# Kernel tuning notes

Measured on AMD Instinct MI355X. Metric: run time of the kernel, lower is better.

The kernel has to match this reference:

```python
import jax, jax.numpy as jnp
import numpy as np

B = 4096      # batch
IN = 512      # input_size
HS = [256, 128, 64]  # hidden_sizes (num liquid neurons per layer)
S = 64        # liquid_state_size
OUT = 12      # output_size


def setup_inputs() -> dict:
    key = jax.random.key(0)
    keys = iter(jax.random.split(key, 40))

    def rn(shape, scale=0.05):
        return jax.random.normal(next(keys), shape, dtype=jnp.float32) * scale

    inp = {"x": jax.random.normal(next(keys), (B, IN), dtype=jnp.float32)}
    sizes = [IN] + HS
    for l, (din, n) in enumerate(zip(sizes[:-1], sizes[1:])):
        inp[f"Wi{l}"] = rn((n, din, S))   # stacked input_projection weights
        inp[f"bi{l}"] = rn((n, S))        # input_projection biases
        inp[f"bl{l}"] = rn((n, S))        # liquid_state biases (hidden starts at 0)
        inp[f"Wo{l}"] = rn((n, S))        # output_projection weights (out dim 1)
        inp[f"bo{l}"] = rn((n,))          # output_projection biases
        inp[f"L{l}"]  = rn((n, n), 0.1)   # lateral_weights
        inp[f"a{l}"]  = jnp.ones((n,), jnp.float32)  # adaptation_state
    inp["Wout"] = rn((HS[-1], OUT))
    inp["bout"] = rn((OUT,))
    return inp


def _liquid_layer(x, Wi, bi, bl, Wo, bo, L, a):
    # Stacked over neurons n: liquid_input[b,n,s] = x @ Wi_n + bi_n + bl_n
    li = jnp.einsum('bi,nis->bns', x, Wi) + bi[None] + bl[None]
    act = jnp.tanh(li) + 0.1 * jnp.sin(0.5 * li) * jnp.cos(0.3 * li)
    # per-neuron scalar output projection -> [B, N]
    out = jnp.einsum('bns,ns->bn', act, Wo) + bo
    # lateral mixing + adaptation scaling
    out = out + 0.1 * (out @ L)
    return out * a


def reference(x, Wi0, bi0, bl0, Wo0, bo0, L0, a0,
              Wi1, bi1, bl1, Wo1, bo1, L1, a1,
              Wi2, bi2, bl2, Wo2, bo2, L2, a2,
              Wout, bout):
    h = _liquid_layer(x, Wi0, bi0, bl0, Wo0, bo0, L0, a0)
    h = _liquid_layer(h, Wi1, bi1, bl1, Wo1, bo1, L1, a1)
    h = _liquid_layer(h, Wi2, bi2, bl2, Wo2, bo2, L2, a2)
    return h @ Wout + bout
```

## Files before the change

### kernel.cpp

```cpp
#include <hip/hip_runtime.h>
#include <hip/hip_bf16.h>
#include <math.h>


#define BATCH 4096

typedef __bf16 bf16x8 __attribute__((ext_vector_type(8)));
typedef float floatx4 __attribute__((ext_vector_type(4)));

__device__ __forceinline__ void gl_lds16(const void* g, void* l) {
    __builtin_amdgcn_global_load_lds(
        (const __attribute__((address_space(1))) void*)g,
        (__attribute__((address_space(3))) void*)l, 16, 0, 0);
}

__device__ __forceinline__ float act_exact(float v) {
    return tanhf(v) + 0.1f * sinf(0.5f * v) * cosf(0.3f * v);
}


__device__ __forceinline__ void wconv_tile(const float* __restrict__ Wi,
                                           __hip_bfloat16* __restrict__ Wt,
                                           int K, int n, int k0, int t)
{
    __shared__ float lds[64][65];
    const float* src = Wi + ((size_t)n * K + k0) * 64;
#pragma unroll
    for (int i = 0; i < 4; ++i) {
        int idx = t + i * 256;
        int r = idx >> 4;
        int s4 = (idx & 15) * 4;
        float4 v = *(const float4*)(src + (size_t)r * 64 + s4);
        lds[s4 + 0][r] = v.x;
        lds[s4 + 1][r] = v.y;
        lds[s4 + 2][r] = v.z;
        lds[s4 + 3][r] = v.w;
    }
    __syncthreads();
    __hip_bfloat16* dst = Wt + (size_t)n * 64 * K + k0;
#pragma unroll
    for (int i = 0; i < 4; ++i) {
        int idx = t + i * 256;
        int s = idx >> 4;
        int k4 = (idx & 15) * 4;
        union { ushort4 u4; __hip_bfloat16 b[4]; } o;
        o.b[0] = __float2bfloat16(lds[s][k4 + 0]);
        o.b[1] = __float2bfloat16(lds[s][k4 + 1]);
        o.b[2] = __float2bfloat16(lds[s][k4 + 2]);
        o.b[3] = __float2bfloat16(lds[s][k4 + 3]);
        *(ushort4*)(dst + (size_t)s * K + k4) = o.u4;
    }
}

__global__ __launch_bounds__(256) void conv_all(
    const float* __restrict__ x, __hip_bfloat16* __restrict__ xb,
    const float* __restrict__ Wi0, const float* __restrict__ Wi1,
    const float* __restrict__ Wi2,
    __hip_bfloat16* __restrict__ Wt0, __hip_bfloat16* __restrict__ Wt1,
    __hip_bfloat16* __restrict__ Wt2, float* __restrict__ Tg)
{
    int bid = blockIdx.x;
    int t = threadIdx.x;
    if (bid < 2048) {
        int g = bid * 256 + t;
        float4 v = ((const float4*)x)[g];
        union { ushort4 u4; __hip_bfloat16 b[4]; } o;
        o.b[0] = __float2bfloat16(v.x);
        o.b[1] = __float2bfloat16(v.y);
        o.b[2] = __float2bfloat16(v.z);
        o.b[3] = __float2bfloat16(v.w);
        ((ushort4*)xb)[g] = o.u4;
    } else if (bid < 4096) {
        int r = bid - 2048;
        wconv_tile(Wi0, Wt0, 512, r >> 3, (r & 7) * 64, t);
    } else if (bid < 4608) {
        int r = bid - 4096;
        wconv_tile(Wi1, Wt1, 256, r >> 2, (r & 3) * 64, t);
    } else if (bid < 4736) {
        int r = bid - 4608;
        wconv_tile(Wi2, Wt2, 128, r >> 1, (r & 1) * 64, t);
    } else {
#pragma unroll
        for (int i = 0; i < 2; ++i) {
            int e = t + 256 * i;
            float v0 = (float)(e - 256) * 0.03125f;
            Tg[2 * e] = act_exact(v0);
            Tg[2 * e + 1] = act_exact(v0 + 0.03125f);
        }
    }
}


__global__ __launch_bounds__(512, 4) void liquid_proj_mfma(
    const __hip_bfloat16* __restrict__ X,
    const __hip_bfloat16* __restrict__ Wt,
    const float* __restrict__ bi, const float* __restrict__ bl,
    const float* __restrict__ Wo, const float* __restrict__ bo,
    const float* __restrict__ Tg,
    __hip_bfloat16* __restrict__ t, int K, int Nn)
{
    __shared__ __align__(16) __hip_bfloat16 As[128 * 64];
    __shared__ __align__(16) __hip_bfloat16 Bs[256 * 64];
    __shared__ __align__(16) float Tt[1024];

    const int tid = threadIdx.x;
    const int wid = tid >> 6;
    const int wb = wid & 1;
    const int wn = wid >> 1;
    const int lane = tid & 63;
    const int m = lane & 15;
    const int qd = lane >> 4;

    const int bid = blockIdx.x;
    const int xcd = bid & 7;
    const int sw = bid >> 3;
    const int n_grp = sw >> 2;
    const int row_grp = ((sw & 3) << 3) | xcd;
    const int row0 = row_grp * 128;
    const int n0 = n_grp * 4;
    const int n = n0 + wn;

    if (tid < 256)
        gl_lds16(Tg + tid * 4, (void*)(Tt + tid * 4));

    floatx4 acc[4][4];
#pragma unroll
    for (int rt = 0; rt < 4; ++rt) {
        int sb = n * 64 + rt * 16 + qd * 4;
        float4 b4i = *(const float4*)(bi + sb);
        float4 b4l = *(const float4*)(bl + sb);
        floatx4 b4 = {b4i.x + b4l.x, b4i.y + b4l.y, b4i.z + b4l.z, b4i.w + b4l.w};
#pragma unroll
        for (int ct = 0; ct < 4; ++ct)
            acc[rt][ct] = b4;
    }

    const int ar0 = tid >> 3;
    const int aq0 = (tid & 7) ^ (ar0 & 7);
    const int ar1 = (tid + 512) >> 3;
    const int aq1 = ((tid + 512) & 7) ^ (ar1 & 7);
    const __hip_bfloat16* Xr0 = X + (size_t)(row0 + ar0) * K + aq0 * 8;
    const __hip_bfloat16* Xr1 = X + (size_t)(row0 + ar1) * K + aq1 * 8;

    const __hip_bfloat16* bsrc[4];
#pragma unroll
    for (int i = 0; i < 4; ++i) {
        int Li = i * 512 + tid;
        int c = Li >> 3;
        int q = (Li & 7) ^ (c & 7);
        bsrc[i] = Wt + ((size_t)(n0 + (c >> 6)) * 64 + (c & 63)) * K + q * 8;
    }

    for (int k0 = 0; k0 < K; k0 += 64) {
        gl_lds16(Xr0 + k0, (void*)(As + tid * 8));
        gl_lds16(Xr1 + k0, (void*)(As + ((size_t)tid + 512) * 8));
#pragma unroll
        for (int i = 0; i < 4; ++i)
            gl_lds16(bsrc[i] + k0, (void*)(Bs + ((size_t)i * 512 + tid) * 8));
        __syncthreads();
#pragma unroll
        for (int kk = 0; kk < 2; ++kk) {
            bf16x8 af[4], bfr[4];
#pragma unroll
            for (int rt = 0; rt < 4; ++rt) {
                int sr = wn * 64 + rt * 16 + m;
                int slot = sr * 8 + ((kk * 4 + qd) ^ (sr & 7));
                af[rt] = *(const bf16x8*)(Bs + slot * 8);
            }
#pragma unroll
            for (int ct = 0; ct < 4; ++ct) {
                int br = wb * 64 + ct * 16 + m;
                int slot = br * 8 + ((kk * 4 + qd) ^ (br & 7));
                bfr[ct] = *(const bf16x8*)(As + slot * 8);
            }
#pragma unroll
            for (int rt = 0; rt < 4; ++rt)
#pragma unroll
                for (int ct = 0; ct < 4; ++ct)
                    acc[rt][ct] = __builtin_amdgcn_mfma_f32_16x16x32_bf16(
                        af[rt], bfr[ct], acc[rt][ct], 0, 0, 0);
        }
        __syncthreads();
    }

    float wo[4][4];
#pragma unroll
    for (int rt = 0; rt < 4; ++rt) {
        float4 w4 = *(const float4*)(Wo + n * 64 + rt * 16 + qd * 4);
        wo[rt][0] = w4.x; wo[rt][1] = w4.y; wo[rt][2] = w4.z; wo[rt][3] = w4.w;
    }
    float bov = bo[n];
    float p[4] = {0.f, 0.f, 0.f, 0.f};
    const float2* Tt2 = (const float2*)Tt;
#pragma unroll
    for (int ct = 0; ct < 4; ++ct)
#pragma unroll
        for (int rt = 0; rt < 4; ++rt)
#pragma unroll
            for (int reg = 0; reg < 4; ++reg) {
                float v = acc[rt][ct][reg];
                float u = fmaf(v, 32.f, 256.f);
                u = fminf(fmaxf(u, 0.f), 510.99f);
                float fi = floorf(u);
                int ii = (int)fi;
                float fr = u - fi;
                float2 pr = Tt2[ii];
                p[ct] = fmaf(fmaf(fr, pr.y - pr.x, pr.x), wo[rt][reg], p[ct]);
            }
#pragma unroll
    for (int ct = 0; ct < 4; ++ct) {
        p[ct] += __shfl_xor(p[ct], 16, 64);
        p[ct] += __shfl_xor(p[ct], 32, 64);
    }
    if (qd == 0) {
#pragma unroll
        for (int ct = 0; ct < 4; ++ct)
            t[(size_t)(row0 + wb * 64 + ct * 16 + m) * Nn + n] =
                __float2bfloat16(p[ct] + bov);
    }
}


template <int NN, int NNSH, bool FINAL>
__global__ __launch_bounds__(256) void lateral_fused(
    const __hip_bfloat16* __restrict__ t,
    const float* __restrict__ Lm,
    const float* __restrict__ a,
    __hip_bfloat16* __restrict__ h,
    const float* __restrict__ Wout,
    const float* __restrict__ bout,
    float* __restrict__ y)
{
    constexpr int RPT = NN / 16;
    __shared__ float tbT[NN][20];
    __shared__ float hb[16][65];

    const int tid = threadIdx.x;
    const int row0 = blockIdx.x * 16;

#pragma unroll
    for (int i = 0; i < NN / 16; ++i) {
        int idx = tid + i * 256;
        int r = idx >> NNSH;
        int c = idx & (NN - 1);
        tbT[c][r] = __bfloat162float(t[(size_t)(row0 + r) * NN + c]);
    }
    __syncthreads();

    const int c = tid & (NN - 1);
    const int rb = (tid >> NNSH) * RPT;
    float acc[RPT];
#pragma unroll
    for (int r = 0; r < RPT; ++r) acc[r] = 0.f;

    for (int mm = 0; mm < NN; ++mm) {
        float lv = Lm[mm * NN + c];
#pragma unroll
        for (int rr = 0; rr < RPT / 4; ++rr) {
            float4 tv = *(const float4*)&tbT[mm][rb + 4 * rr];
            acc[4 * rr + 0] += tv.x * lv;
            acc[4 * rr + 1] += tv.y * lv;
            acc[4 * rr + 2] += tv.z * lv;
            acc[4 * rr + 3] += tv.w * lv;
        }
    }
    float av = a[c];
#pragma unroll
    for (int r = 0; r < RPT; ++r) {
        float hv = (tbT[c][rb + r] + 0.1f * acc[r]) * av;
        if constexpr (FINAL) {
            hb[rb + r][c] = hv;
        } else {
            h[(size_t)(row0 + rb + r) * NN + c] = __float2bfloat16(hv);
        }
    }
    if constexpr (FINAL) {
        __syncthreads();
        if (tid < 192) {
            int r = tid / 12, o = tid - 12 * r;
            float accy = bout[o];
#pragma unroll
            for (int k = 0; k < 64; ++k)
                accy += hb[r][k] * Wout[k * 12 + o];
            y[(size_t)(row0 + r) * 12 + o] = accy;
        }
    }
}


__global__ __launch_bounds__(256) void liquid_proj_f32(
    const float* __restrict__ x, const float* __restrict__ Wi,
    const float* __restrict__ bi, const float* __restrict__ bl,
    const float* __restrict__ Wo, const float* __restrict__ bo,
    float* __restrict__ t, int K, int Nn)
{
    __shared__ float xs[16][65];
    __shared__ float ws[16][65];
    const int tid = threadIdx.x;
    const int tx = tid & 15, ty = tid >> 4;
    const int row0 = blockIdx.x * 64;
    const int n = blockIdx.y;
    const float* Wn = Wi + (size_t)n * K * 64;
    float acc[4][4] = {};
    for (int k0 = 0; k0 < K; k0 += 16) {
#pragma unroll
        for (int i = 0; i < 4; ++i) {
            int li = tid + 256 * i;
            xs[li & 15][li >> 4] = x[(size_t)(row0 + (li >> 4)) * K + k0 + (li & 15)];
        }
#pragma unroll
        for (int i = 0; i < 4; ++i) {
            int li = tid + 256 * i;
            ws[li >> 6][li & 63] = Wn[(size_t)(k0 + (li >> 6)) * 64 + (li & 63)];
        }
        __syncthreads();
#pragma unroll
        for (int kk = 0; kk < 16; ++kk) {
            float xa[4], wb[4];
#pragma unroll
            for (int i = 0; i < 4; ++i) xa[i] = xs[kk][4 * ty + i];
#pragma unroll
            for (int j = 0; j < 4; ++j) wb[j] = ws[kk][4 * tx + j];
#pragma unroll
            for (int i = 0; i < 4; ++i)
#pragma unroll
                for (int j = 0; j < 4; ++j) acc[i][j] += xa[i] * wb[j];
        }
        __syncthreads();
    }
    float part[4] = {0.f, 0.f, 0.f, 0.f};
#pragma unroll
    for (int j = 0; j < 4; ++j) {
        int cc = 4 * tx + j;
        float bias = bi[n * 64 + cc] + bl[n * 64 + cc];
        float wov = Wo[n * 64 + cc];
#pragma unroll
        for (int i = 0; i < 4; ++i) {
            float v = acc[i][j] + bias;
            part[i] += (tanhf(v) + 0.1f * sinf(0.5f * v) * cosf(0.3f * v)) * wov;
        }
    }
#pragma unroll
    for (int mk = 1; mk < 16; mk <<= 1)
#pragma unroll
        for (int i = 0; i < 4; ++i) part[i] += __shfl_xor(part[i], mk, 64);
    if (tx == 0) {
        float b = bo[n];
#pragma unroll
        for (int i = 0; i < 4; ++i)
            t[(size_t)(row0 + 4 * ty + i) * Nn + n] = part[i] + b;
    }
}

__global__ void lateral_f32_kernel(const float* __restrict__ t,
                                   const float* __restrict__ L,
                                   const float* __restrict__ a,
                                   float* __restrict__ h, int Nn)
{
    extern __shared__ float tb[];
    const int b = blockIdx.x;
    const int n = threadIdx.x;
    tb[n] = t[(size_t)b * Nn + n];
    __syncthreads();
    float acc = 0.f;
    for (int mm = 0; mm < Nn; ++mm)
        acc += tb[mm] * L[(size_t)mm * Nn + n];
    h[(size_t)b * Nn + n] = (tb[n] + 0.1f * acc) * a[n];
}

__global__ void out_f32_kernel(const float* __restrict__ h,
                               const float* __restrict__ Wout,
                               const float* __restrict__ bout,
                               float* __restrict__ y)
{
    int g = blockIdx.x * blockDim.x + threadIdx.x;
    if (g >= BATCH * 12) return;
    int b = g / 12, o = g - 12 * b;
    float acc = bout[o];
    const float* hb = h + (size_t)b * 64;
#pragma unroll
    for (int k = 0; k < 64; ++k) acc += hb[k] * Wout[k * 12 + o];
    y[g] = acc;
}

extern "C" void kernel_launch(void* const* d_in, const int* in_sizes, int n_in,
                              void* d_out, int out_size, void* d_ws, size_t ws_size,
                              hipStream_t stream)
{
    (void)in_sizes; (void)n_in; (void)out_size;
    const float* x = (const float*)d_in[0];
    const float* Wout = (const float*)d_in[22];
    const float* bout = (const float*)d_in[23];
    const int dims[4] = {512, 256, 128, 64};
    char* ws = (char*)d_ws;
    const size_t MB = 1024u * 1024u;

    if (ws_size >= 28 * MB) {
        __hip_bfloat16* Wt0 = (__hip_bfloat16*)ws;
        __hip_bfloat16* Wt1 = (__hip_bfloat16*)(ws + 16 * MB);
        __hip_bfloat16* Wt2 = (__hip_bfloat16*)(ws + 20 * MB);
        __hip_bfloat16* Wts[3] = {Wt0, Wt1, Wt2};
        __hip_bfloat16* xb = (__hip_bfloat16*)(ws + 21 * MB);
        __hip_bfloat16* h0 = xb;
        __hip_bfloat16* h1 = (__hip_bfloat16*)(ws + 23 * MB);
        __hip_bfloat16* tbuf = (__hip_bfloat16*)(ws + 25 * MB);
        float* Tg = (float*)(ws + 27 * MB);

        conv_all<<<4737, 256, 0, stream>>>(
            x, xb, (const float*)d_in[1], (const float*)d_in[8],
            (const float*)d_in[15], Wt0, Wt1, Wt2, Tg);

        const __hip_bfloat16* prev = xb;
        const __hip_bfloat16* hbuf[3] = {h0, h1, nullptr};
        for (int l = 0; l < 3; ++l) {
            const float* bi = (const float*)d_in[1 + 7 * l + 1];
            const float* bl = (const float*)d_in[1 + 7 * l + 2];
            const float* Wo = (const float*)d_in[1 + 7 * l + 3];
            const float* bo = (const float*)d_in[1 + 7 * l + 4];
            const float* L  = (const float*)d_in[1 + 7 * l + 5];
            const float* a  = (const float*)d_in[1 + 7 * l + 6];
            const int K = dims[l], Nn = dims[l + 1];

            liquid_proj_mfma<<<32 * (Nn / 4), 512, 0, stream>>>(
                prev, Wts[l], bi, bl, Wo, bo, Tg, tbuf, K, Nn);
            if (l == 0)
                lateral_fused<256, 8, false><<<BATCH / 16, 256, 0, stream>>>(
                    tbuf, L, a, h0, nullptr, nullptr, nullptr);
            else if (l == 1)
                lateral_fused<128, 7, false><<<BATCH / 16, 256, 0, stream>>>(
                    tbuf, L, a, h1, nullptr, nullptr, nullptr);
            else
                lateral_fused<64, 6, true><<<BATCH / 16, 256, 0, stream>>>(
                    tbuf, L, a, nullptr, Wout, bout, (float*)d_out);
            prev = hbuf[l];
        }
    } else {
        float* tbufs[3] = {(float*)ws, (float*)ws, (float*)(ws + 4 * MB)};
        float* hs[3] = {(float*)(ws + 4 * MB), (float*)(ws + 2 * MB),
                        (float*)(ws + 5 * MB)};
        const float* prev = x;
        for (int l = 0; l < 3; ++l) {
            const float* Wi = (const float*)d_in[1 + 7 * l + 0];
            const float* bi = (const float*)d_in[1 + 7 * l + 1];
            const float* bl = (const float*)d_in[1 + 7 * l + 2];
            const float* Wo = (const float*)d_in[1 + 7 * l + 3];
            const float* bo = (const float*)d_in[1 + 7 * l + 4];
            const float* L  = (const float*)d_in[1 + 7 * l + 5];
            const float* a  = (const float*)d_in[1 + 7 * l + 6];
            const int K = dims[l], Nn = dims[l + 1];
            liquid_proj_f32<<<dim3(BATCH / 64, Nn), 256, 0, stream>>>(
                prev, Wi, bi, bl, Wo, bo, tbufs[l], K, Nn);
            lateral_f32_kernel<<<BATCH, Nn, Nn * sizeof(float), stream>>>(
                tbufs[l], L, a, hs[l], Nn);
            prev = hs[l];
        }
        out_f32_kernel<<<(BATCH * 12 + 255) / 256, 256, 0, stream>>>(
            hs[2], Wout, bout, (float*)d_out);
    }
}
```

Baseline: 268.5 us.

## Double-buffer projection GEMM with 256-row tiles and phased async LDS loads

Replaces the projection MFMA kernel with a templated version that works on 256 batch rows per block instead of 128, doubling per-warp accumulators to 4x8. Each block keeps two LDS stages and issues the global-to-LDS loads for the next K tile in quarters, interleaved with MFMA phases. It uses explicit vmcnt waits, barriers and setprio, so memory latency overlaps compute and the number of X reloads across neuron groups drops. In exchange, LDS and register use per block rises (occupancy bound lowered to 2), the grid gets smaller, and the hand-tuned barrier and waitcnt choreography is fragile.

```diff
diff --git a/kernel.cpp b/kernel.cpp
--- a/kernel.cpp
+++ b/kernel.cpp
@@ -91,16 +91,18 @@
 }
 
 
-__global__ __launch_bounds__(512, 4) void liquid_proj_mfma(
+template <int KT>
+__global__ __launch_bounds__(512, 2) void liquid_proj_mfma8(
     const __hip_bfloat16* __restrict__ X,
     const __hip_bfloat16* __restrict__ Wt,
     const float* __restrict__ bi, const float* __restrict__ bl,
     const float* __restrict__ Wo, const float* __restrict__ bo,
     const float* __restrict__ Tg,
-    __hip_bfloat16* __restrict__ t, int K, int Nn)
-{
-    __shared__ __align__(16) __hip_bfloat16 As[128 * 64];
-    __shared__ __align__(16) __hip_bfloat16 Bs[256 * 64];
+    __hip_bfloat16* __restrict__ out, int Nn)
+{
+    constexpr int NT = KT / 64;
+    __shared__ __align__(16) __hip_bfloat16 Xs[2][256 * 64];
+    __shared__ __align__(16) __hip_bfloat16 Ws[2][256 * 64];
     __shared__ __align__(16) float Tt[1024];
 
     const int tid = threadIdx.x;
@@ -114,16 +116,11 @@
     const int bid = blockIdx.x;
     const int xcd = bid & 7;
     const int sw = bid >> 3;
-    const int n_grp = sw >> 2;
-    const int row_grp = ((sw & 3) << 3) | xcd;
-    const int row0 = row_grp * 128;
-    const int n0 = n_grp * 4;
+    const int row0 = ((((sw & 1) << 3) | xcd)) << 8;
+    const int n0 = (sw >> 1) << 2;
     const int n = n0 + wn;
 
-    if (tid < 256)
-        gl_lds16(Tg + tid * 4, (void*)(Tt + tid * 4));
-
-    floatx4 acc[4][4];
+    floatx4 acc[4][8];
 #pragma unroll
     for (int rt = 0; rt < 4; ++rt) {
         int sb = n * 64 + rt * 16 + qd * 4;
@@ -131,56 +128,92 @@
         float4 b4l = *(const float4*)(bl + sb);
         floatx4 b4 = {b4i.x + b4l.x, b4i.y + b4l.y, b4i.z + b4l.z, b4i.w + b4l.w};
 #pragma unroll
-        for (int ct = 0; ct < 4; ++ct)
+        for (int ct = 0; ct < 8; ++ct)
             acc[rt][ct] = b4;
     }
 
-    const int ar0 = tid >> 3;
-    const int aq0 = (tid & 7) ^ (ar0 & 7);
-    const int ar1 = (tid + 512) >> 3;
-    const int aq1 = ((tid + 512) & 7) ^ (ar1 & 7);
-    const __hip_bfloat16* Xr0 = X + (size_t)(row0 + ar0) * K + aq0 * 8;
-    const __hip_bfloat16* Xr1 = X + (size_t)(row0 + ar1) * K + aq1 * 8;
-
-    const __hip_bfloat16* bsrc[4];
-#pragma unroll
-    for (int i = 0; i < 4; ++i) {
-        int Li = i * 512 + tid;
-        int c = Li >> 3;
-        int q = (Li & 7) ^ (c & 7);
-        bsrc[i] = Wt + ((size_t)(n0 + (c >> 6)) * 64 + (c & 63)) * K + q * 8;
-    }
-
-    for (int k0 = 0; k0 < K; k0 += 64) {
-        gl_lds16(Xr0 + k0, (void*)(As + tid * 8));
-        gl_lds16(Xr1 + k0, (void*)(As + ((size_t)tid + 512) * 8));
-#pragma unroll
-        for (int i = 0; i < 4; ++i)
-            gl_lds16(bsrc[i] + k0, (void*)(Bs + ((size_t)i * 512 + tid) * 8));
-        __syncthreads();
-#pragma unroll
-        for (int kk = 0; kk < 2; ++kk) {
-            bf16x8 af[4], bfr[4];
-#pragma unroll
-            for (int rt = 0; rt < 4; ++rt) {
-                int sr = wn * 64 + rt * 16 + m;
-                int slot = sr * 8 + ((kk * 4 + qd) ^ (sr & 7));
-                af[rt] = *(const bf16x8*)(Bs + slot * 8);
+    if (tid < 256)
+        gl_lds16(Tg + tid * 4, (void*)(Tt + tid * 4));
+
+    const int srow = tid >> 3;
+    const int q8 = (tid & 7) ^ (srow & 7);
+    const __hip_bfloat16* Ax = X + (size_t)(row0 + srow) * KT + q8 * 8;
+    const __hip_bfloat16* Bw = Wt + ((size_t)n0 * 64 + srow) * KT + q8 * 8;
+
+    auto stX = [&](int d, int h, int tt) {
+        gl_lds16(Ax + (size_t)(h * 128) * KT + tt * 64,
+                 (void*)(Xs[d] + ((size_t)h * 1024 + tid) * 8));
+        gl_lds16(Ax + (size_t)(h * 128 + 64) * KT + tt * 64,
+                 (void*)(Xs[d] + ((size_t)h * 1024 + 512 + tid) * 8));
+    };
+    auto stW = [&](int d, int h, int tt) {
+        gl_lds16(Bw + (size_t)(h * 128) * KT + tt * 64,
+                 (void*)(Ws[d] + ((size_t)h * 1024 + tid) * 8));
+        gl_lds16(Bw + (size_t)(h * 128 + 64) * KT + tt * 64,
+                 (void*)(Ws[d] + ((size_t)h * 1024 + 512 + tid) * 8));
+    };
+
+    stX(0, 0, 0); stX(0, 1, 0); stW(0, 0, 0); stW(0, 1, 0);
+    stX(1, 0, 1); stX(1, 1, 1); stW(1, 0, 1); stW(1, 1, 1);
+    asm volatile("s_waitcnt vmcnt(8)" ::: "memory");
+    __builtin_amdgcn_sched_barrier(0);
+    __builtin_amdgcn_s_barrier();
+
+#pragma unroll
+    for (int t = 0; t < NT; ++t) {
+        const int cur = t & 1;
+        const int nxt = cur ^ 1;
+        bf16x8 af[4][2];
+#pragma unroll
+        for (int p = 0; p < 4; ++p) {
+            if (p == 0) {
+#pragma unroll
+                for (int rt = 0; rt < 4; ++rt) {
+                    int r = wn * 64 + rt * 16 + m;
+#pragma unroll
+                    for (int kk = 0; kk < 2; ++kk)
+                        af[rt][kk] = *(const bf16x8*)(
+                            Ws[cur] + ((size_t)r * 8 + ((kk * 4 + qd) ^ (r & 7))) * 8);
+                }
             }
-#pragma unroll
-            for (int ct = 0; ct < 4; ++ct) {
-                int br = wb * 64 + ct * 16 + m;
-                int slot = br * 8 + ((kk * 4 + qd) ^ (br & 7));
-                bfr[ct] = *(const bf16x8*)(As + slot * 8);
+            bf16x8 bfr[2][2];
+#pragma unroll
+            for (int ctl = 0; ctl < 2; ++ctl) {
+                int r = wb * 128 + (2 * p + ctl) * 16 + m;
+#pragma unroll
+                for (int kk = 0; kk < 2; ++kk)
+                    bfr[ctl][kk] = *(const bf16x8*)(
+                        Xs[cur] + ((size_t)r * 8 + ((kk * 4 + qd) ^ (r & 7))) * 8);
             }
-#pragma unroll
-            for (int rt = 0; rt < 4; ++rt)
-#pragma unroll
-                for (int ct = 0; ct < 4; ++ct)
-                    acc[rt][ct] = __builtin_amdgcn_mfma_f32_16x16x32_bf16(
-                        af[rt], bfr[ct], acc[rt][ct], 0, 0, 0);
-        }
-        __syncthreads();
+            if (p == 0 && t >= 1 && t + 1 < NT) stX(nxt, 0, t + 1);
+            if (p == 1 && t >= 1 && t + 1 < NT) stX(nxt, 1, t + 1);
+            if (p == 2 && t + 2 < NT) stW(cur, 0, t + 2);
+            if (p == 3 && t + 2 < NT) stW(cur, 1, t + 2);
+
+            __builtin_amdgcn_s_barrier();
+            asm volatile("s_waitcnt lgkmcnt(0)" ::: "memory");
+            __builtin_amdgcn_sched_barrier(0);
+            __builtin_amdgcn_s_setprio(1);
+#pragma unroll
+            for (int ctl = 0; ctl < 2; ++ctl)
+#pragma unroll
+                for (int rt = 0; rt < 4; ++rt)
+#pragma unroll
+                    for (int kk = 0; kk < 2; ++kk)
+                        acc[rt][2 * p + ctl] = __builtin_amdgcn_mfma_f32_16x16x32_bf16(
+                            af[rt][kk], bfr[ctl][kk], acc[rt][2 * p + ctl], 0, 0, 0);
+            __builtin_amdgcn_s_setprio(0);
+
+            if (p == 3 && t + 1 < NT) {
+                if (t + 2 < NT)
+                    asm volatile("s_waitcnt vmcnt(4)" ::: "memory");
+                else
+                    asm volatile("s_waitcnt vmcnt(0)" ::: "memory");
+                __builtin_amdgcn_sched_barrier(0);
+            }
+            if (!(p == 3 && t + 1 == NT))
+                __builtin_amdgcn_s_barrier();
+        }
     }
 
     float wo[4][4];
@@ -189,11 +222,11 @@
         float4 w4 = *(const float4*)(Wo + n * 64 + rt * 16 + qd * 4);
         wo[rt][0] = w4.x; wo[rt][1] = w4.y; wo[rt][2] = w4.z; wo[rt][3] = w4.w;
     }
-    float bov = bo[n];
-    float p[4] = {0.f, 0.f, 0.f, 0.f};
+    const float bov = bo[n];
+    float p8[8] = {0.f, 0.f, 0.f, 0.f, 0.f, 0.f, 0.f, 0.f};
     const float2* Tt2 = (const float2*)Tt;
 #pragma unroll
-    for (int ct = 0; ct < 4; ++ct)
+    for (int ct = 0; ct < 8; ++ct)
 #pragma unroll
         for (int rt = 0; rt < 4; ++rt)
 #pragma unroll
@@ -205,18 +238,18 @@
                 int ii = (int)fi;
                 float fr = u - fi;
                 float2 pr = Tt2[ii];
-                p[ct] = fmaf(fmaf(fr, pr.y - pr.x, pr.x), wo[rt][reg], p[ct]);
+                p8[ct] = fmaf(fmaf(fr, pr.y - pr.x, pr.x), wo[rt][reg], p8[ct]);
             }
 #pragma unroll
-    for (int ct = 0; ct < 4; ++ct) {
-        p[ct] += __shfl_xor(p[ct], 16, 64);
-        p[ct] += __shfl_xor(p[ct], 32, 64);
+    for (int ct = 0; ct < 8; ++ct) {
+        p8[ct] += __shfl_xor(p8[ct], 16, 64);
+        p8[ct] += __shfl_xor(p8[ct], 32, 64);
     }
     if (qd == 0) {
 #pragma unroll
-        for (int ct = 0; ct < 4; ++ct)
-            t[(size_t)(row0 + wb * 64 + ct * 16 + m) * Nn + n] =
-                __float2bfloat16(p[ct] + bov);
+        for (int ct = 0; ct < 8; ++ct)
+            out[(size_t)(row0 + wb * 128 + ct * 16 + m) * Nn + n] =
+                __float2bfloat16(p8[ct] + bov);
     }
 }
 
@@ -419,10 +452,17 @@
             const float* bo = (const float*)d_in[1 + 7 * l + 4];
             const float* L  = (const float*)d_in[1 + 7 * l + 5];
             const float* a  = (const float*)d_in[1 + 7 * l + 6];
-            const int K = dims[l], Nn = dims[l + 1];
-
-            liquid_proj_mfma<<<32 * (Nn / 4), 512, 0, stream>>>(
-                prev, Wts[l], bi, bl, Wo, bo, Tg, tbuf, K, Nn);
+
+            if (l == 0)
+                liquid_proj_mfma8<512><<<16 * 64, 512, 0, stream>>>(
+                    prev, Wts[0], bi, bl, Wo, bo, Tg, tbuf, 256);
+            else if (l == 1)
+                liquid_proj_mfma8<256><<<16 * 32, 512, 0, stream>>>(
+                    prev, Wts[1], bi, bl, Wo, bo, Tg, tbuf, 128);
+            else
+                liquid_proj_mfma8<128><<<16 * 16, 512, 0, stream>>>(
+                    prev, Wts[2], bi, bl, Wo, bo, Tg, tbuf, 64);
+
             if (l == 0)
                 lateral_fused<256, 8, false><<<BATCH / 16, 256, 0, stream>>>(
                     tbuf, L, a, h0, nullptr, nullptr, nullptr);
```

After: 290.0 us. 8.0% more time.

## Fold lateral mixing and adaptation into next layer's input weights

Applied to the files above, without the earlier changes.

The lateral mix (I + 0.1 L) and the adaptation scale a are linear, so they are folded into the next layer's projection weights: W' = diag(a) Wi + 0.1 L (diag(a) Wi), computed once per call by a new small MFMA GEMM kernel. Layers 0 and 1 then feed their raw projection outputs straight into the next layer's GEMM, which removes two lateral_fused launches and their intermediate buffers. The cost is an extra weight-folding GEMM each call and extra bf16 rounding of the folded weights and of L.

```diff
diff --git a/kernel.cpp b/kernel.cpp
--- a/kernel.cpp
+++ b/kernel.cpp
@@ -21,6 +21,7 @@
 
 __device__ __forceinline__ void wconv_tile(const float* __restrict__ Wi,
                                            __hip_bfloat16* __restrict__ Wt,
+                                           const float* __restrict__ a,
                                            int K, int n, int k0, int t)
 {
     __shared__ float lds[64][65];
@@ -31,6 +32,10 @@
         int r = idx >> 4;
         int s4 = (idx & 15) * 4;
         float4 v = *(const float4*)(src + (size_t)r * 64 + s4);
+        if (a) {
+            float av = a[k0 + r];
+            v.x *= av; v.y *= av; v.z *= av; v.w *= av;
+        }
         lds[s4 + 0][r] = v.x;
         lds[s4 + 1][r] = v.y;
         lds[s4 + 2][r] = v.z;
@@ -56,8 +61,12 @@
     const float* __restrict__ x, __hip_bfloat16* __restrict__ xb,
     const float* __restrict__ Wi0, const float* __restrict__ Wi1,
     const float* __restrict__ Wi2,
-    __hip_bfloat16* __restrict__ Wt0, __hip_bfloat16* __restrict__ Wt1,
-    __hip_bfloat16* __restrict__ Wt2, float* __restrict__ Tg)
+    const float* __restrict__ a0, const float* __restrict__ a1,
+    const float* __restrict__ L0, const float* __restrict__ L1,
+    __hip_bfloat16* __restrict__ Wt0, __hip_bfloat16* __restrict__ G1,
+    __hip_bfloat16* __restrict__ G2,
+    __hip_bfloat16* __restrict__ Lb0, __hip_bfloat16* __restrict__ Lb1,
+    float* __restrict__ Tg)
 {
     int bid = blockIdx.x;
     int t = threadIdx.x;
@@ -72,14 +81,14 @@
         ((ushort4*)xb)[g] = o.u4;
     } else if (bid < 4096) {
         int r = bid - 2048;
-        wconv_tile(Wi0, Wt0, 512, r >> 3, (r & 7) * 64, t);
+        wconv_tile(Wi0, Wt0, nullptr, 512, r >> 3, (r & 7) * 64, t);
     } else if (bid < 4608) {
         int r = bid - 4096;
-        wconv_tile(Wi1, Wt1, 256, r >> 2, (r & 3) * 64, t);
+        wconv_tile(Wi1, G1, a0, 256, r >> 2, (r & 3) * 64, t);
     } else if (bid < 4736) {
         int r = bid - 4608;
-        wconv_tile(Wi2, Wt2, 128, r >> 1, (r & 1) * 64, t);
-    } else {
+        wconv_tile(Wi2, G2, a1, 128, r >> 1, (r & 1) * 64, t);
+    } else if (bid == 4736) {
 #pragma unroll
         for (int i = 0; i < 2; ++i) {
             int e = t + 256 * i;
@@ -87,6 +96,24 @@
             Tg[2 * e] = act_exact(v0);
             Tg[2 * e + 1] = act_exact(v0 + 0.03125f);
         }
+    } else if (bid < 4801) {
+        int g = (bid - 4737) * 1024 + t * 4;
+        float4 v = *(const float4*)(L0 + g);
+        union { ushort4 u4; __hip_bfloat16 b[4]; } o;
+        o.b[0] = __float2bfloat16(v.x);
+        o.b[1] = __float2bfloat16(v.y);
+        o.b[2] = __float2bfloat16(v.z);
+        o.b[3] = __float2bfloat16(v.w);
+        *(ushort4*)(Lb0 + g) = o.u4;
+    } else {
+        int g = (bid - 4801) * 1024 + t * 4;
+        float4 v = *(const float4*)(L1 + g);
+        union { ushort4 u4; __hip_bfloat16 b[4]; } o;
+        o.b[0] = __float2bfloat16(v.x);
+        o.b[1] = __float2bfloat16(v.y);
+        o.b[2] = __float2bfloat16(v.z);
+        o.b[3] = __float2bfloat16(v.w);
+        *(ushort4*)(Lb1 + g) = o.u4;
     }
 }
 
@@ -221,6 +248,106 @@
 }
 
 
+__global__ __launch_bounds__(512, 4) void fold_lateral(
+    const __hip_bfloat16* __restrict__ G1, const __hip_bfloat16* __restrict__ Lb0,
+    __hip_bfloat16* __restrict__ W1,
+    const __hip_bfloat16* __restrict__ G2, const __hip_bfloat16* __restrict__ Lb1,
+    __hip_bfloat16* __restrict__ W2)
+{
+    __shared__ __align__(16) __hip_bfloat16 As[128 * 64];
+    __shared__ __align__(16) __hip_bfloat16 Bs[256 * 64];
+
+    const int bid = blockIdx.x;
+    const __hip_bfloat16* G;
+    const __hip_bfloat16* Lb;
+    __hip_bfloat16* W;
+    int r0, e0, K;
+    if (bid < 64) {
+        G = G1; Lb = Lb0; W = W1; K = 256;
+        r0 = (bid >> 1) * 256; e0 = (bid & 1) * 128;
+    } else {
+        G = G2; Lb = Lb1; W = W2; K = 128;
+        r0 = (bid - 64) * 256; e0 = 0;
+    }
+
+    const int tid = threadIdx.x;
+    const int wid = tid >> 6;
+    const int wb = wid & 1;
+    const int wn = wid >> 1;
+    const int lane = tid & 63;
+    const int m = lane & 15;
+    const int qd = lane >> 4;
+
+    floatx4 acc[4][4];
+#pragma unroll
+    for (int rt = 0; rt < 4; ++rt)
+#pragma unroll
+        for (int ct = 0; ct < 4; ++ct)
+            acc[rt][ct] = {0.f, 0.f, 0.f, 0.f};
+
+    const int ar0 = tid >> 3;
+    const int aq0 = (tid & 7) ^ (ar0 & 7);
+    const int ar1 = (tid + 512) >> 3;
+    const int aq1 = ((tid + 512) & 7) ^ (ar1 & 7);
+    const __hip_bfloat16* Xr0 = Lb + (size_t)(e0 + ar0) * K + aq0 * 8;
+    const __hip_bfloat16* Xr1 = Lb + (size_t)(e0 + ar1) * K + aq1 * 8;
+
+    const __hip_bfloat16* bsrc[4];
+#pragma unroll
+    for (int i = 0; i < 4; ++i) {
+        int Li = i * 512 + tid;
+        int c = Li >> 3;
+        int q = (Li & 7) ^ (c & 7);
+        bsrc[i] = G + (size_t)(r0 + c) * K + q * 8;
+    }
+
+    for (int k0 = 0; k0 < K; k0 += 64) {
+        gl_lds16(Xr0 + k0, (void*)(As + tid * 8));
+        gl_lds16(Xr1 + k0, (void*)(As + ((size_t)tid + 512) * 8));
+#pragma unroll
+        for (int i = 0; i < 4; ++i)
+            gl_lds16(bsrc[i] + k0, (void*)(Bs + ((size_t)i * 512 + tid) * 8));
+        __syncthreads();
+#pragma unroll
+        for (int kk = 0; kk < 2; ++kk) {
+            bf16x8 af[4], bfr[4];
+#pragma unroll
+            for (int rt = 0; rt < 4; ++rt) {
+                int sr = wn * 64 + rt * 16 + m;
+                int slot = sr * 8 + ((kk * 4 + qd) ^ (sr & 7));
+                af[rt] = *(const bf16x8*)(Bs + slot * 8);
+            }
+#pragma unroll
+            for (int ct = 0; ct < 4; ++ct) {
+                int br = wb * 64 + ct * 16 + m;
+                int slot = br * 8 + ((kk * 4 + qd) ^ (br & 7));
+                bfr[ct] = *(const bf16x8*)(As + slot * 8);
+            }
+#pragma unroll
+            for (int rt = 0; rt < 4; ++rt)
+#pragma unroll
+                for (int ct = 0; ct < 4; ++ct)
+                    acc[rt][ct] = __builtin_amdgcn_mfma_f32_16x16x32_bf16(
+                        af[rt], bfr[ct], acc[rt][ct], 0, 0, 0);
+        }
+        __syncthreads();
+    }
+
+#pragma unroll
+    for (int rt = 0; rt < 4; ++rt)
+#pragma unroll
+        for (int ct = 0; ct < 4; ++ct)
+#pragma unroll
+            for (int reg = 0; reg < 4; ++reg) {
+                int rl = wn * 64 + rt * 16 + qd * 4 + reg;
+                int el = wb * 64 + ct * 16 + m;
+                size_t gi = (size_t)(r0 + rl) * K + (e0 + el);
+                W[gi] = __float2bfloat16(
+                    __bfloat162float(G[gi]) + 0.1f * acc[rt][ct][reg]);
+            }
+}
+
+
 template <int NN, int NNSH, bool FINAL>
 __global__ __launch_bounds__(256) void lateral_fused(
     const __hip_bfloat16* __restrict__ t,
@@ -394,46 +521,49 @@
     const int dims[4] = {512, 256, 128, 64};
     char* ws = (char*)d_ws;
     const size_t MB = 1024u * 1024u;
+    const size_t KB = 1024u;
 
     if (ws_size >= 28 * MB) {
         __hip_bfloat16* Wt0 = (__hip_bfloat16*)ws;
-        __hip_bfloat16* Wt1 = (__hip_bfloat16*)(ws + 16 * MB);
-        __hip_bfloat16* Wt2 = (__hip_bfloat16*)(ws + 20 * MB);
-        __hip_bfloat16* Wts[3] = {Wt0, Wt1, Wt2};
-        __hip_bfloat16* xb = (__hip_bfloat16*)(ws + 21 * MB);
-        __hip_bfloat16* h0 = xb;
-        __hip_bfloat16* h1 = (__hip_bfloat16*)(ws + 23 * MB);
-        __hip_bfloat16* tbuf = (__hip_bfloat16*)(ws + 25 * MB);
+        __hip_bfloat16* G1  = (__hip_bfloat16*)(ws + 16 * MB);
+        __hip_bfloat16* G2  = (__hip_bfloat16*)(ws + 20 * MB);
+        __hip_bfloat16* xb  = (__hip_bfloat16*)(ws + 21 * MB);
+        __hip_bfloat16* W1f = (__hip_bfloat16*)(ws + 21 * MB);
+        __hip_bfloat16* t0  = (__hip_bfloat16*)(ws + 25 * MB);
+        __hip_bfloat16* t1  = (__hip_bfloat16*)ws;
+        __hip_bfloat16* W2f = (__hip_bfloat16*)(ws + 2 * MB);
+        __hip_bfloat16* t2  = (__hip_bfloat16*)(ws + 4 * MB);
         float* Tg = (float*)(ws + 27 * MB);
-
-        conv_all<<<4737, 256, 0, stream>>>(
+        __hip_bfloat16* Lb0 = (__hip_bfloat16*)(ws + 27 * MB + 16 * KB);
+        __hip_bfloat16* Lb1 = (__hip_bfloat16*)(ws + 27 * MB + 160 * KB);
+
+        const float* a0 = (const float*)d_in[7];
+        const float* a1 = (const float*)d_in[14];
+        const float* L0 = (const float*)d_in[6];
+        const float* L1 = (const float*)d_in[13];
+
+        conv_all<<<4817, 256, 0, stream>>>(
             x, xb, (const float*)d_in[1], (const float*)d_in[8],
-            (const float*)d_in[15], Wt0, Wt1, Wt2, Tg);
-
-        const __hip_bfloat16* prev = xb;
-        const __hip_bfloat16* hbuf[3] = {h0, h1, nullptr};
-        for (int l = 0; l < 3; ++l) {
-            const float* bi = (const float*)d_in[1 + 7 * l + 1];
-            const float* bl = (const float*)d_in[1 + 7 * l + 2];
-            const float* Wo = (const float*)d_in[1 + 7 * l + 3];
-            const float* bo = (const float*)d_in[1 + 7 * l + 4];
-            const float* L  = (const float*)d_in[1 + 7 * l + 5];
-            const float* a  = (const float*)d_in[1 + 7 * l + 6];
-            const int K = dims[l], Nn = dims[l + 1];
-
-            liquid_proj_mfma<<<32 * (Nn / 4), 512, 0, stream>>>(
-                prev, Wts[l], bi, bl, Wo, bo, Tg, tbuf, K, Nn);
-            if (l == 0)
-                lateral_fused<256, 8, false><<<BATCH / 16, 256, 0, stream>>>(
-                    tbuf, L, a, h0, nullptr, nullptr, nullptr);
-            else if (l == 1)
-                lateral_fused<128, 7, false><<<BATCH / 16, 256, 0, stream>>>(
-                    tbuf, L, a, h1, nullptr, nullptr, nullptr);
-            else
-                lateral_fused<64, 6, true><<<BATCH / 16, 256, 0, stream>>>(
-                    tbuf, L, a, nullptr, Wout, bout, (float*)d_out);
-            prev = hbuf[l];
-        }
+            (const float*)d_in[15], a0, a1, L0, L1,
+            Wt0, G1, G2, Lb0, Lb1, Tg);
+
+        liquid_proj_mfma<<<32 * 64, 512, 0, stream>>>(
+            xb, Wt0, (const float*)d_in[2], (const float*)d_in[3],
+            (const float*)d_in[4], (const float*)d_in[5], Tg, t0, 512, 256);
+
+        fold_lateral<<<80, 512, 0, stream>>>(G1, Lb0, W1f, G2, Lb1, W2f);
+
+        liquid_proj_mfma<<<32 * 32, 512, 0, stream>>>(
+            t0, W1f, (const float*)d_in[9], (const float*)d_in[10],
+            (const float*)d_in[11], (const float*)d_in[12], Tg, t1, 256, 128);
+
+        liquid_proj_mfma<<<32 * 16, 512, 0, stream>>>(
+            t1, W2f, (const float*)d_in[16], (const float*)d_in[17],
+            (const float*)d_in[18], (const float*)d_in[19], Tg, t2, 128, 64);
+
+        lateral_fused<64, 6, true><<<BATCH / 16, 256, 0, stream>>>(
+            t2, (const float*)d_in[20], (const float*)d_in[21],
+            nullptr, Wout, bout, (float*)d_out);
     } else {
         float* tbufs[3] = {(float*)ws, (float*)ws, (float*)(ws + 4 * MB)};
         float* hs[3] = {(float*)(ws + 4 * MB), (float*)(ws + 2 * MB),
```

New measurement: 254.1 us. 5.4% less time.
